# Optimization experiments

Measured on AMD Instinct MI355X. Metric: run time of the kernel, lower is better.

The kernel has to match this reference:

```python
import jax, jax.numpy as jnp
import numpy as np

H = 8
HD = 16  # head_dim = out_features // n_heads = 128 // 8


def setup_inputs() -> dict:
    key = jax.random.key(0)
    k1, k2, k3, k4, k5 = jax.random.split(key, 5)
    B, N, F_IN, F_OUT = 4, 2048, 128, 128
    x = jax.random.normal(k1, (B, N, F_IN), dtype=jnp.float32)
    adj = jax.random.randint(k2, (B, N, N), 0, 2, dtype=jnp.int32)
    W = jax.random.normal(k3, (F_IN, F_OUT), dtype=jnp.float32) * (1.0 / np.sqrt(F_IN))
    a = jax.random.normal(k4, (H, 2 * HD), dtype=jnp.float32) * 0.1
    Wo = jax.random.normal(k5, (F_OUT, F_OUT), dtype=jnp.float32) * (1.0 / np.sqrt(F_OUT))
    bo = jnp.zeros((F_OUT,), dtype=jnp.float32)
    return {"x": x, "adj": adj, "W": W, "a": a, "Wo": Wo, "bo": bo}


def reference(x, adj, W, a, Wo, bo):
    B, N, _ = x.shape
    # Linear projection (no bias), split heads: [B,H,N,HD]
    Wx = (x @ W).reshape(B, N, H, HD).transpose(0, 2, 1, 3)
    # Additive attention scores: e_ij = leaky(a_l . Wx_i + a_r . Wx_j)
    e_i = jnp.einsum('bhnd,hd->bhn', Wx, a[:, :HD])  # [B,H,N]
    e_j = jnp.einsum('bhnd,hd->bhn', Wx, a[:, HD:])  # [B,H,N]
    e = jax.nn.leaky_relu(e_i[:, :, :, None] + e_j[:, :, None, :], negative_slope=0.2)
    # Mask to edges of adj; rows with no edges -> all -inf -> softmax NaN -> 0
    mask = (adj[:, None, :, :] == 0)  # [B,1,N,N] broadcast over heads
    e = jnp.where(mask, -jnp.inf, e)
    attn = jax.nn.softmax(e, axis=-1)
    attn = jnp.nan_to_num(attn, nan=0.0)
    # Weighted aggregation, merge heads: [B,N,F_OUT]
    h = jnp.einsum('bhij,bhjd->bhid', attn, Wx)
    h = h.transpose(0, 2, 1, 3).reshape(B, N, H * HD)
    # out_proj (nn.Linear: y = h @ Wo.T + bo) then ELU
    return jax.nn.elu(h @ Wo.T + bo)
```

## Files before the change

### kernel.cpp

```cpp
#include <hip/hip_runtime.h>
#include <hip/hip_bf16.h>
#include <cstdint>


typedef float f32x2 __attribute__((ext_vector_type(2)));
typedef float f32x4 __attribute__((ext_vector_type(4)));
typedef __bf16 bf16x8 __attribute__((ext_vector_type(8)));
typedef unsigned long long u64;

__device__ __forceinline__ float lsel(float v, u64 m, u64 lanebit) {
#if __has_builtin(__builtin_amdgcn_inverse_ballot_w64)
    (void)lanebit;
    return __builtin_amdgcn_inverse_ballot_w64(m) ? v : 0.0f;
#else
    return (m & lanebit) ? v : 0.0f;
#endif
}

__global__ __launch_bounds__(256)
void prep_kernel(const float* __restrict__ x, const float* __restrict__ W,
                 const float* __restrict__ a, const float* __restrict__ Wo,
                 const int* __restrict__ adj,
                 unsigned short* __restrict__ vfrag,
                 float2* __restrict__ EI, float2* __restrict__ EJ2,
                 float* __restrict__ WoT,
                 u64* __restrict__ tmask)
{
    const int t = threadIdx.x;

    if (blockIdx.x < 2048) {
        __shared__ int al[16][257];
        const int blk2 = blockIdx.x;
        const int b = blk2 >> 9;
        const int tile = (blk2 >> 2) & 127;
        const int jq = blk2 & 3;
        const int rowbase = b * 2048 + tile * 16;
        const int w = t >> 6, lane = t & 63;
        const int r = lane & 15, jg = lane >> 4;
        const int srow = t >> 4, scol = (t & 15) * 16;

        #pragma unroll
        for (int cc = 0; cc < 2; ++cc) {
            const int jc = jq * 512 + cc * 256;
            const int* gsrc = adj + (size_t)(rowbase + srow) * 2048 + jc + scol;
            #pragma unroll
            for (int q = 0; q < 4; ++q) {
                const int4 v = *reinterpret_cast<const int4*>(&gsrc[q * 4]);
                al[srow][scol + q * 4 + 0] = v.x;
                al[srow][scol + q * 4 + 1] = v.y;
                al[srow][scol + q * 4 + 2] = v.z;
                al[srow][scol + q * 4 + 3] = v.w;
            }
            __syncthreads();
            u64 myw = 0;
            #pragma unroll
            for (int kk = 0; kk < 2; ++kk) {
                const int c0 = w * 64 + kk * 32 + jg * 8;
                const int4 a0 = *reinterpret_cast<const int4*>(&al[r][c0]);
                const int4 a1 = *reinterpret_cast<const int4*>(&al[r][c0 + 4]);
                const int av[8] = {a0.x, a0.y, a0.z, a0.w, a1.x, a1.y, a1.z, a1.w};
                #pragma unroll
                for (int e = 0; e < 8; ++e) {
                    const u64 bal = __ballot(av[e] != 0);
                    const int widx = kk * 8 + e;
                    if (lane == widx) myw = bal;
                }
            }
            __syncthreads();
            const int jtw = jq * 8 + cc * 4 + w;
            if (lane < 16)
                tmask[((size_t)(b * 128 + tile) * 32 + jtw) * 16 + lane] = myw;
        }
        return;
    }

    const int blk = blockIdx.x - 2048;
    if (blk == 1024) {
        if (t < 128)
            for (int k = 0; k < 128; ++k)
                WoT[k * 128 + t] = Wo[t * 128 + k];
        return;
    }
    __shared__ float xl[8 * 128];
    __shared__ float xw[8 * 128];
    const int row0 = blk * 8;
    if (t < 128) {
        #pragma unroll
        for (int r = 0; r < 8; ++r)
            xl[r * 128 + t] = x[(size_t)(row0 + r) * 128 + t];
    }
    __syncthreads();

    if (t < 128) {
        float acc[8] = {0.f, 0.f, 0.f, 0.f, 0.f, 0.f, 0.f, 0.f};
        for (int k = 0; k < 128; k += 4) {
            const float w0 = W[(k + 0) * 128 + t];
            const float w1 = W[(k + 1) * 128 + t];
            const float w2 = W[(k + 2) * 128 + t];
            const float w3 = W[(k + 3) * 128 + t];
            #pragma unroll
            for (int r = 0; r < 8; ++r) {
                const float4 xv = *reinterpret_cast<const float4*>(&xl[r * 128 + k]);
                acc[r] += xv.x * w0 + xv.y * w1 + xv.z * w2 + xv.w * w3;
            }
        }
        #pragma unroll
        for (int r = 0; r < 8; ++r) xw[r * 128 + t] = acc[r];
    }
    __syncthreads();

    if (t < 128) {
        const int b = row0 >> 11, n0 = row0 & 2047;
        bf16x8 st;
        #pragma unroll
        for (int r = 0; r < 8; ++r) st[r] = (__bf16)xw[r * 128 + t];
        const int hh = t >> 4, rr = t & 15;
        const int w32 = n0 >> 5, jgp = (n0 >> 3) & 3;
        *reinterpret_cast<bf16x8*>(
            &vfrag[(((size_t)(b * 8 + hh) * 64 + w32) * 64 + jgp * 16 + rr) * 8]) = st;

        const int r = t >> 4, h = (t >> 1) & 7, s = t & 1;
        float dot = 0.f;
        #pragma unroll
        for (int d = 0; d < 16; ++d)
            dot += xw[r * 128 + h * 16 + d] * a[h * 32 + s * 16 + d];
        float2 ev; ev.x = __expf(dot); ev.y = __expf(0.2f * dot);
        const int idx = (b * 8 + h) * 2048 + n0 + r;
        if (s) EJ2[idx] = ev; else EI[idx] = ev;
    }
}

__global__ __launch_bounds__(256, 6)
void gat_part(const u64* __restrict__ tmask,
              const unsigned short* __restrict__ vfrag,
              const float2* __restrict__ EI, const float2* __restrict__ EJ2,
              float* __restrict__ pacc, float* __restrict__ psum)
{
    const int tid = threadIdx.x;
    const int hw = tid >> 6;
    const int lane = tid & 63;
    const int r = lane & 15;
    const int jg = lane >> 4;
    const u64 lanebit = 1ull << lane;
    const int x = blockIdx.x & 7, w = blockIdx.x >> 3;
    const int tg = x * 64 + (w & 63);
    const int sub = w >> 6;
    const int jh = sub >> 1, hg = sub & 1;
    const int b = tg >> 7;
    const int tile = tg & 127;
    const int ibase = tile << 4;
    const int h = hg * 4 + hw;

    __shared__ __align__(16) float2 EjL[2][4][128];

    const int eb = (b * 8 + h) * 2048;
    const float2 q0 = EI[eb + ibase + r];
    f32x2 Eipk; Eipk[0] = q0.x; Eipk[1] = q0.y;
    const u64* tmrow = tmask + (size_t)(b * 128 + tile) * 512;
    const unsigned short* vfr = vfrag + (size_t)(b * 8 + h) * 64 * 64 * 8;
    const float2* EJ2G = EJ2 + eb;

    f32x4 acc  = {0.f, 0.f, 0.f, 0.f};
    f32x4 accS = {0.f, 0.f, 0.f, 0.f};
    bf16x8 ones;
    #pragma unroll
    for (int e2 = 0; e2 < 8; ++e2) ones[e2] = (__bf16)1.0f;

    const int jbase = jh * 1024;
    const int wbase = jh * 32;

    bf16x8 vC0, vC1, vC2, vC3, vN0, vN1, vN2, vN3;
    vC0 = *reinterpret_cast<const bf16x8*>(&vfr[((wbase + 0) * 64 + lane) * 8]);
    vC1 = *reinterpret_cast<const bf16x8*>(&vfr[((wbase + 1) * 64 + lane) * 8]);
    vC2 = *reinterpret_cast<const bf16x8*>(&vfr[((wbase + 2) * 64 + lane) * 8]);
    vC3 = *reinterpret_cast<const bf16x8*>(&vfr[((wbase + 3) * 64 + lane) * 8]);
    {
        const float4 s0 = *reinterpret_cast<const float4*>(&EJ2G[jbase + lane * 2]);
        *reinterpret_cast<float4*>(&EjL[0][hw][lane * 2]) = s0;
    }
    __syncthreads();

    int cur = 0;
    for (int c = 0; c < 8; ++c) {
        const int cn = (c + 1) & 7;
        const int w32n = wbase + cn * 4;
        const int jn = jbase + cn * 128;
        vN0 = *reinterpret_cast<const bf16x8*>(&vfr[((w32n + 0) * 64 + lane) * 8]);
        vN1 = *reinterpret_cast<const bf16x8*>(&vfr[((w32n + 1) * 64 + lane) * 8]);
        vN2 = *reinterpret_cast<const bf16x8*>(&vfr[((w32n + 2) * 64 + lane) * 8]);
        vN3 = *reinterpret_cast<const bf16x8*>(&vfr[((w32n + 3) * 64 + lane) * 8]);
        const float4 snq = *reinterpret_cast<const float4*>(&EJ2G[jn + lane * 2]);
        __builtin_amdgcn_sched_barrier(0);

        const u64* tmw = tmrow + (jh * 16 + c * 2) * 16;
        u64 mwA[16], mwB[16];
        #pragma unroll
        for (int e2 = 0; e2 < 16; ++e2) mwA[e2] = tmw[e2];
        #pragma unroll
        for (int e2 = 0; e2 < 16; ++e2) mwB[e2] = tmw[16 + e2];

        #pragma unroll
        for (int kk = 0; kk < 4; ++kk) {
            const float2* ejp = &EjL[cur][hw][kk * 32 + jg * 8];
            const bf16x8 v = (kk == 0) ? vC0 : (kk == 1) ? vC1 : (kk == 2) ? vC2 : vC3;
            const u64* mwp = (kk < 2) ? mwA : mwB;
            const int mof = (kk & 1) * 8;
            bf16x8 afr;
            #pragma unroll
            for (int e2 = 0; e2 < 8; ++e2) {
                const float2 q = ejp[e2];
                f32x2 tq; tq[0] = q.x; tq[1] = q.y;
                const f32x2 tt = Eipk * tq;
                const float p = fmaxf(tt[0], tt[1]);
                afr[e2] = (__bf16)lsel(p, mwp[mof + e2], lanebit);
            }
            acc  = __builtin_amdgcn_mfma_f32_16x16x32_bf16(afr, v,    acc,  0, 0, 0);
            accS = __builtin_amdgcn_mfma_f32_16x16x32_bf16(afr, ones, accS, 0, 0, 0);
        }

        const int nb = cur ^ 1;
        *reinterpret_cast<float4*>(&EjL[nb][hw][lane * 2]) =
            *reinterpret_cast<const float4*>(&snq);
        __syncthreads();
        vC0 = vN0; vC1 = vN1; vC2 = vN2; vC3 = vN3;
        cur = nb;
    }

    const size_t pb = (size_t)((b * 128 + tile) * 2 + jh);
    float* pa = pacc + pb * 2048;
    float* ps = psum + pb * 128;
    #pragma unroll
    for (int q = 0; q < 4; ++q) {
        const int row = jg * 4 + q;
        pa[row * 128 + hg * 64 + hw * 16 + r] = acc[q];
        if (r == 0) ps[(hg * 4 + hw) * 16 + row] = accS[q];
    }
}

__global__ __launch_bounds__(256)
void combine_kernel(const float* __restrict__ pacc, const float* __restrict__ psum,
                    const float* __restrict__ WoT, const float* __restrict__ bo,
                    float* __restrict__ out)
{
    const int tid = threadIdx.x;
    const int bid = (blockIdx.x & 7) * 64 + (blockIdx.x >> 3);
    const int b = bid >> 7;
    const int tile = bid & 127;
    const int ibase = tile << 4;

    __shared__ float hl[16][128];
    const size_t pb0 = (size_t)((b * 128 + tile) * 2);
    const float* pa0 = pacc + pb0 * 2048;
    const float* pa1 = pa0 + 2048;
    const float* ps0 = psum + pb0 * 128;
    const float* ps1 = ps0 + 128;

    #pragma unroll
    for (int k = 0; k < 8; ++k) {
        const int idx = k * 256 + tid;
        const int row = idx >> 7, f = idx & 127, h = f >> 4;
        const float num = pa0[idx] + pa1[idx];
        const float den = ps0[h * 16 + row] + ps1[h * 16 + row];
        const float inv = (den > 0.f) ? 1.f / den : 0.f;
        hl[row][f] = num * inv;
    }
    __syncthreads();

    const int f = tid & 127;
    const int rg = tid >> 7;
    float o[8] = {0.f, 0.f, 0.f, 0.f, 0.f, 0.f, 0.f, 0.f};
    for (int k = 0; k < 128; k += 4) {
        const float w0 = WoT[(k + 0) * 128 + f];
        const float w1 = WoT[(k + 1) * 128 + f];
        const float w2 = WoT[(k + 2) * 128 + f];
        const float w3 = WoT[(k + 3) * 128 + f];
        #pragma unroll
        for (int q = 0; q < 8; ++q) {
            const float4 hv = *reinterpret_cast<const float4*>(&hl[rg * 8 + q][k]);
            o[q] += hv.x * w0 + hv.y * w1 + hv.z * w2 + hv.w * w3;
        }
    }
    const float bv = bo[f];
    #pragma unroll
    for (int q = 0; q < 8; ++q) {
        float v = o[q] + bv;
        v = (v > 0.f) ? v : (__expf(v) - 1.f);
        out[(size_t)(b * 2048 + ibase + rg * 8 + q) * 128 + f] = v;
    }
}

extern "C" void kernel_launch(void* const* d_in, const int* in_sizes, int n_in,
                              void* d_out, int out_size, void* d_ws, size_t ws_size,
                              hipStream_t stream) {
    const float* x   = (const float*)d_in[0];
    const int*   adj = (const int*)d_in[1];
    const float* W   = (const float*)d_in[2];
    const float* a   = (const float*)d_in[3];
    const float* Wo  = (const float*)d_in[4];
    const float* bo  = (const float*)d_in[5];
    float* out = (float*)d_out;

    char* ws = (char*)d_ws;
    unsigned short* vfrag = (unsigned short*)ws;
    float2* EI  = (float2*)(ws + (size_t)2 * 1024 * 1024);
    float2* EJ2 = EI + 4 * 8 * 2048;
    float* WoT  = (float*)(EJ2 + 4 * 8 * 2048);
    u64* tmask = (u64*)(WoT + 128 * 128);
    float* pacc = (float*)(tmask + (size_t)512 * 512);
    float* psum = pacc + (size_t)1024 * 2048;

    prep_kernel<<<dim3(2048 + 1025), dim3(256), 0, stream>>>(
        x, W, a, Wo, adj, vfrag, EI, EJ2, WoT, tmask);
    gat_part<<<dim3(2048), dim3(256), 0, stream>>>(
        tmask, vfrag, EI, EJ2, pacc, psum);
    combine_kernel<<<dim3(512), dim3(256), 0, stream>>>(
        pacc, psum, WoT, bo, out);
}
```

Before: 70.64 us.

## Split Ej planes, add vfrag shuffle kernel, pack attention-weight math with inline asm

Stores the exp(e_j) and exp(0.2 e_j) values in separate planar arrays so the attention loop can read them as float4 from shared memory. It then computes two j columns at once with v_pk_mul_f32 and packs the results to bf16 pairs with v_cvt_pk_bf16_f32. The prep kernel now writes Wx transposed with coalesced stores, and a new shuffle kernel rearranges it into the MFMA fragment layout, replacing the old scattered stores. The goal is fewer VALU and LDS instructions in the hot loop, at the cost of an extra kernel launch and an extra pass over the Wx buffer.

```diff
diff --git a/kernel.cpp b/kernel.cpp
--- a/kernel.cpp
+++ b/kernel.cpp
@@ -16,13 +16,24 @@
     return (m & lanebit) ? v : 0.0f;
 #endif
 }
+__device__ __forceinline__ f32x2 pkmul(f32x2 a, f32x2 b) {
+    f32x2 d;
+    asm("v_pk_mul_f32 %0, %1, %2" : "=v"(d) : "v"(a), "v"(b));
+    return d;
+}
+__device__ __forceinline__ unsigned cvtpk(float lo, float hi) {
+    unsigned d;
+    asm("v_cvt_pk_bf16_f32 %0, %1, %2" : "=v"(d) : "v"(lo), "v"(hi));
+    return d;
+}
 
 __global__ __launch_bounds__(256)
 void prep_kernel(const float* __restrict__ x, const float* __restrict__ W,
                  const float* __restrict__ a, const float* __restrict__ Wo,
                  const int* __restrict__ adj,
-                 unsigned short* __restrict__ vfrag,
-                 float2* __restrict__ EI, float2* __restrict__ EJ2,
+                 unsigned short* __restrict__ wxT,
+                 float2* __restrict__ EI,
+                 float* __restrict__ EjT, float* __restrict__ Ej5T,
                  float* __restrict__ WoT,
                  u64* __restrict__ tmask)
 {
@@ -114,26 +125,42 @@
         bf16x8 st;
         #pragma unroll
         for (int r = 0; r < 8; ++r) st[r] = (__bf16)xw[r * 128 + t];
-        const int hh = t >> 4, rr = t & 15;
-        const int w32 = n0 >> 5, jgp = (n0 >> 3) & 3;
-        *reinterpret_cast<bf16x8*>(
-            &vfrag[(((size_t)(b * 8 + hh) * 64 + w32) * 64 + jgp * 16 + rr) * 8]) = st;
+        *reinterpret_cast<bf16x8*>(&wxT[((size_t)(b * 128 + t)) * 2048 + n0]) = st;
 
         const int r = t >> 4, h = (t >> 1) & 7, s = t & 1;
         float dot = 0.f;
         #pragma unroll
         for (int d = 0; d < 16; ++d)
             dot += xw[r * 128 + h * 16 + d] * a[h * 32 + s * 16 + d];
-        float2 ev; ev.x = __expf(dot); ev.y = __expf(0.2f * dot);
+        const float ef  = __expf(dot);
+        const float ef5 = __expf(0.2f * dot);
         const int idx = (b * 8 + h) * 2048 + n0 + r;
-        if (s) EJ2[idx] = ev; else EI[idx] = ev;
-    }
+        if (s) { EjT[idx] = ef; Ej5T[idx] = ef5; }
+        else   { float2 ev; ev.x = ef; ev.y = ef5; EI[idx] = ev; }
+    }
+}
+
+__global__ __launch_bounds__(256)
+void vshuf_kernel(const unsigned short* __restrict__ wxT,
+                  unsigned short* __restrict__ vfrag)
+{
+    const int gid = blockIdx.x * 256 + threadIdx.x;
+    const int lane = gid & 63;
+    const int w32 = (gid >> 6) & 63;
+    const int bh = gid >> 12;
+    const int b = bh >> 3, h = bh & 7;
+    const int f = h * 16 + (lane & 15);
+    const int j = w32 * 32 + (lane >> 4) * 8;
+    const bf16x8 v = *reinterpret_cast<const bf16x8*>(
+        &wxT[((size_t)(b * 128 + f)) * 2048 + j]);
+    *reinterpret_cast<bf16x8*>(&vfrag[(size_t)gid * 8]) = v;
 }
 
 __global__ __launch_bounds__(256, 6)
 void gat_part(const u64* __restrict__ tmask,
               const unsigned short* __restrict__ vfrag,
-              const float2* __restrict__ EI, const float2* __restrict__ EJ2,
+              const float2* __restrict__ EI,
+              const float* __restrict__ EjT, const float* __restrict__ Ej5T,
               float* __restrict__ pacc, float* __restrict__ psum)
 {
     const int tid = threadIdx.x;
@@ -151,14 +178,18 @@
     const int ibase = tile << 4;
     const int h = hg * 4 + hw;
 
-    __shared__ __align__(16) float2 EjL[2][4][128];
+    __shared__ __align__(16) float EjL[2][4][128];
+    __shared__ __align__(16) float Ej5L[2][4][128];
 
     const int eb = (b * 8 + h) * 2048;
     const float2 q0 = EI[eb + ibase + r];
-    f32x2 Eipk; Eipk[0] = q0.x; Eipk[1] = q0.y;
+    f32x2 EiE, Ei5E;
+    EiE[0] = q0.x;  EiE[1] = q0.x;
+    Ei5E[0] = q0.y; Ei5E[1] = q0.y;
     const u64* tmrow = tmask + (size_t)(b * 128 + tile) * 512;
     const unsigned short* vfr = vfrag + (size_t)(b * 8 + h) * 64 * 64 * 8;
-    const float2* EJ2G = EJ2 + eb;
+    const float* EjG  = EjT  + eb;
+    const float* Ej5G = Ej5T + eb;
 
     f32x4 acc  = {0.f, 0.f, 0.f, 0.f};
     f32x4 accS = {0.f, 0.f, 0.f, 0.f};
@@ -175,8 +206,10 @@
     vC2 = *reinterpret_cast<const bf16x8*>(&vfr[((wbase + 2) * 64 + lane) * 8]);
     vC3 = *reinterpret_cast<const bf16x8*>(&vfr[((wbase + 3) * 64 + lane) * 8]);
     {
-        const float4 s0 = *reinterpret_cast<const float4*>(&EJ2G[jbase + lane * 2]);
-        *reinterpret_cast<float4*>(&EjL[0][hw][lane * 2]) = s0;
+        const float2 s0 = *reinterpret_cast<const float2*>(&EjG[jbase + lane * 2]);
+        const float2 s1 = *reinterpret_cast<const float2*>(&Ej5G[jbase + lane * 2]);
+        *reinterpret_cast<float2*>(&EjL[0][hw][lane * 2]) = s0;
+        *reinterpret_cast<float2*>(&Ej5L[0][hw][lane * 2]) = s1;
     }
     __syncthreads();
 
@@ -189,7 +222,8 @@
         vN1 = *reinterpret_cast<const bf16x8*>(&vfr[((w32n + 1) * 64 + lane) * 8]);
         vN2 = *reinterpret_cast<const bf16x8*>(&vfr[((w32n + 2) * 64 + lane) * 8]);
         vN3 = *reinterpret_cast<const bf16x8*>(&vfr[((w32n + 3) * 64 + lane) * 8]);
-        const float4 snq = *reinterpret_cast<const float4*>(&EJ2G[jn + lane * 2]);
+        const float2 sn  = *reinterpret_cast<const float2*>(&EjG[jn + lane * 2]);
+        const float2 sn5 = *reinterpret_cast<const float2*>(&Ej5G[jn + lane * 2]);
         __builtin_amdgcn_sched_barrier(0);
 
         const u64* tmw = tmrow + (jh * 16 + c * 2) * 16;
@@ -201,26 +235,38 @@
 
         #pragma unroll
         for (int kk = 0; kk < 4; ++kk) {
-            const float2* ejp = &EjL[cur][hw][kk * 32 + jg * 8];
+            const int jloc = kk * 32 + jg * 8;
+            const float4 e0 = *reinterpret_cast<const float4*>(&EjL[cur][hw][jloc]);
+            const float4 e1 = *reinterpret_cast<const float4*>(&EjL[cur][hw][jloc + 4]);
+            const float4 f0 = *reinterpret_cast<const float4*>(&Ej5L[cur][hw][jloc]);
+            const float4 f1 = *reinterpret_cast<const float4*>(&Ej5L[cur][hw][jloc + 4]);
             const bf16x8 v = (kk == 0) ? vC0 : (kk == 1) ? vC1 : (kk == 2) ? vC2 : vC3;
             const u64* mwp = (kk < 2) ? mwA : mwB;
             const int mof = (kk & 1) * 8;
-            bf16x8 afr;
+            const float ee[8] = {e0.x, e0.y, e0.z, e0.w, e1.x, e1.y, e1.z, e1.w};
+            const float ff[8] = {f0.x, f0.y, f0.z, f0.w, f1.x, f1.y, f1.z, f1.w};
+            unsigned au[4];
             #pragma unroll
-            for (int e2 = 0; e2 < 8; ++e2) {
-                const float2 q = ejp[e2];
-                f32x2 tq; tq[0] = q.x; tq[1] = q.y;
-                const f32x2 tt = Eipk * tq;
-                const float p = fmaxf(tt[0], tt[1]);
-                afr[e2] = (__bf16)lsel(p, mwp[mof + e2], lanebit);
+            for (int q = 0; q < 4; ++q) {
+                f32x2 ejp;  ejp[0]  = ee[2 * q]; ejp[1]  = ee[2 * q + 1];
+                f32x2 ej5p; ej5p[0] = ff[2 * q]; ej5p[1] = ff[2 * q + 1];
+                const f32x2 t1 = pkmul(ejp, EiE);
+                const f32x2 t2 = pkmul(ej5p, Ei5E);
+                const float m0 = fmaxf(t1[0], t2[0]);
+                const float m1 = fmaxf(t1[1], t2[1]);
+                const float p0 = lsel(m0, mwp[mof + 2 * q],     lanebit);
+                const float p1 = lsel(m1, mwp[mof + 2 * q + 1], lanebit);
+                au[q] = cvtpk(p0, p1);
             }
-            acc  = __builtin_amdgcn_mfma_f32_16x16x32_bf16(afr, v,    acc,  0, 0, 0);
-            accS = __builtin_amdgcn_mfma_f32_16x16x32_bf16(afr, ones, accS, 0, 0, 0);
+            union { unsigned u[4]; bf16x8 v8; } cvt;
+            cvt.u[0] = au[0]; cvt.u[1] = au[1]; cvt.u[2] = au[2]; cvt.u[3] = au[3];
+            acc  = __builtin_amdgcn_mfma_f32_16x16x32_bf16(cvt.v8, v,    acc,  0, 0, 0);
+            accS = __builtin_amdgcn_mfma_f32_16x16x32_bf16(cvt.v8, ones, accS, 0, 0, 0);
         }
 
         const int nb = cur ^ 1;
-        *reinterpret_cast<float4*>(&EjL[nb][hw][lane * 2]) =
-            *reinterpret_cast<const float4*>(&snq);
+        *reinterpret_cast<float2*>(&EjL[nb][hw][lane * 2]) = sn;
+        *reinterpret_cast<float2*>(&Ej5L[nb][hw][lane * 2]) = sn5;
         __syncthreads();
         vC0 = vN0; vC1 = vN1; vC2 = vN2; vC3 = vN3;
         cur = nb;
@@ -301,18 +347,21 @@
     float* out = (float*)d_out;
 
     char* ws = (char*)d_ws;
-    unsigned short* vfrag = (unsigned short*)ws;
+    unsigned short* wxT = (unsigned short*)ws;
     float2* EI  = (float2*)(ws + (size_t)2 * 1024 * 1024);
-    float2* EJ2 = EI + 4 * 8 * 2048;
-    float* WoT  = (float*)(EJ2 + 4 * 8 * 2048);
+    float* EjT  = (float*)(EI + 4 * 8 * 2048);
+    float* Ej5T = EjT + 4 * 8 * 2048;
+    float* WoT  = Ej5T + 4 * 8 * 2048;
     u64* tmask = (u64*)(WoT + 128 * 128);
-    float* pacc = (float*)(tmask + (size_t)512 * 512);
+    unsigned short* vfrag = (unsigned short*)(tmask + (size_t)512 * 512);
+    float* pacc = (float*)(vfrag + (size_t)1024 * 1024);
     float* psum = pacc + (size_t)1024 * 2048;
 
     prep_kernel<<<dim3(2048 + 1025), dim3(256), 0, stream>>>(
-        x, W, a, Wo, adj, vfrag, EI, EJ2, WoT, tmask);
+        x, W, a, Wo, adj, wxT, EI, EjT, Ej5T, WoT, tmask);
+    vshuf_kernel<<<dim3(512), dim3(256), 0, stream>>>(wxT, vfrag);
     gat_part<<<dim3(2048), dim3(256), 0, stream>>>(
-        tmask, vfrag, EI, EJ2, pacc, psum);
+        tmask, vfrag, EI, EjT, Ej5T, pacc, psum);
     combine_kernel<<<dim3(512), dim3(256), 0, stream>>>(
         pacc, psum, WoT, bo, out);
 }
```

Result: slower. 79.56 us (+12.6%).
